# Kernel tuning notes

Measured on AMD Instinct MI355X. Metric: run time of the kernel, lower is better.

The kernel has to match this reference:

```python
import jax, jax.numpy as jnp
from jax import lax
import numpy as np

NODE_COUNT = 4096
BATCH = 128
THRESHOLD = 1.0
DISSIPATION = 0.1
SPARSITY = 0.9
MAX_ITERS = 100


def setup_inputs() -> dict:
    key = jax.random.key(0)
    k_in, k_conn, k_mask, k_w, k_b = jax.random.split(key, 5)
    input_data = jax.random.normal(k_in, (BATCH, NODE_COUNT), dtype=jnp.float32)
    conn = jax.random.normal(k_conn, (NODE_COUNT, NODE_COUNT), dtype=jnp.float32)
    mask = (jax.random.uniform(k_mask, (NODE_COUNT, NODE_COUNT)) > SPARSITY).astype(jnp.float32)
    conn = conn * mask
    conn = conn / (jnp.abs(conn).sum(axis=1, keepdims=True) + 1e-6)
    # input_proj: Linear(node_count, node_count), torch default init scale
    bound = 1.0 / np.sqrt(NODE_COUNT)
    W = jax.random.uniform(k_w, (NODE_COUNT, NODE_COUNT), minval=-bound, maxval=bound, dtype=jnp.float32)
    b = jax.random.uniform(k_b, (NODE_COUNT,), minval=-bound, maxval=bound, dtype=jnp.float32)
    return {"input_data": input_data, "W": W, "b": b, "connections": conn}


def _avalanche(state, connections):
    """Batched avalanche scan with per-sample sticky early-exit (torch break)."""
    B = state.shape[0]
    done0 = jnp.zeros((B,), dtype=bool)
    total0 = jnp.zeros((B,), dtype=state.dtype)

    def step(carry, _):
        state, done, total = carry
        active = (state > THRESHOLD).astype(state.dtype)          # [B, N]
        n_active = active.sum(axis=1)                              # [B]
        new_done = done | (n_active == 0)                          # break condition
        total = total + jnp.where(new_done, 0.0, n_active)
        # propagated = connections @ active  (per sample)
        prop = jnp.einsum('ij,bj->bi', connections, active)        # [B, N]
        new_state = (state * (1.0 - DISSIPATION) + prop * (1.0 - active)) * (1.0 - active)
        state = jnp.where(new_done[:, None], state, new_state)
        return (state, new_done, total), None

    (state, done, total), _ = lax.scan(step, (state, done0, total0), None, length=MAX_ITERS)
    return state, total


def reference(input_data, W, b, connections):
    projected = input_data @ W.T + b                               # [B, N]
    output, sizes = _avalanche(projected, connections)
    max_size = sizes.max()
    return output, max_size
```

## Files before the change

kernel.cpp:

```cpp
#include <hip/hip_runtime.h>

#define N_NODES 4096
#define BATCH 128
#define SPLITK 8
#define GBN 32
#define PITCH 40
#define KCHUNK (N_NODES / SPLITK)
#define NIT (KCHUNK / 32)
#define GEMM_BLOCKS ((N_NODES / GBN) * SPLITK)
#define TRANS_BLOCKS (64 * 64)

typedef _Float16 f16x4 __attribute__((ext_vector_type(4)));
typedef _Float16 f16x8 __attribute__((ext_vector_type(8)));
typedef float f32x4 __attribute__((ext_vector_type(4)));

#if defined(__has_builtin)
#if __has_builtin(__builtin_amdgcn_cvt_f32_fp8) && __has_builtin(__builtin_amdgcn_cvt_pk_fp8_f32)
#define CONN_FP8 1
#endif
#endif
#ifndef CONN_FP8
#define CONN_FP8 0
#endif

#if CONN_FP8
#define CONN_ELEM_BYTES 1
#define CONN_SCALE (1.0f / 256.0f)
#else
#define CONN_ELEM_BYTES 2
#define CONN_SCALE 1.0f
#endif

__device__ __forceinline__ void conn_store4(void* out, size_t off, float4 v) {
#if CONN_FP8
  unsigned int p = __builtin_amdgcn_cvt_pk_fp8_f32(v.x * 256.0f, v.y * 256.0f, 0, false);
  p = (unsigned int)__builtin_amdgcn_cvt_pk_fp8_f32(v.z * 256.0f, v.w * 256.0f, (int)p, true);
  *(unsigned int*)((unsigned char*)out + off) = p;
#else
  const unsigned int ux = __float_as_uint(v.x), uy = __float_as_uint(v.y);
  const unsigned int uz = __float_as_uint(v.z), uw = __float_as_uint(v.w);
  ushort4 u;
  u.x = (unsigned short)((ux + 0x7FFFu + ((ux >> 16) & 1u)) >> 16);
  u.y = (unsigned short)((uy + 0x7FFFu + ((uy >> 16) & 1u)) >> 16);
  u.z = (unsigned short)((uz + 0x7FFFu + ((uz >> 16) & 1u)) >> 16);
  u.w = (unsigned short)((uw + 0x7FFFu + ((uw >> 16) & 1u)) >> 16);
  *(ushort4*)((unsigned short*)out + off) = u;
#endif
}

__device__ __forceinline__ float4 conn_load4(const void* cT, int j, int t) {
#if CONN_FP8
  const unsigned int c = *(const unsigned int*)((const unsigned char*)cT + ((size_t)j << 12) + t * 4);
  return make_float4(__builtin_amdgcn_cvt_f32_fp8(c, 0), __builtin_amdgcn_cvt_f32_fp8(c, 1),
                     __builtin_amdgcn_cvt_f32_fp8(c, 2), __builtin_amdgcn_cvt_f32_fp8(c, 3));
#else
  const ushort4 c = *(const ushort4*)((const unsigned short*)cT + ((size_t)j << 12) + t * 4);
  return make_float4(__uint_as_float((unsigned int)c.x << 16),
                     __uint_as_float((unsigned int)c.y << 16),
                     __uint_as_float((unsigned int)c.z << 16),
                     __uint_as_float((unsigned int)c.w << 16));
#endif
}

struct GemmSmem {
  alignas(16) _Float16 Ah[2][128 * PITCH];
  alignas(16) _Float16 Al[2][128 * PITCH];
  alignas(16) _Float16 Bh[2][GBN * PITCH];
  alignas(16) _Float16 Bl[2][GBN * PITCH];
};
struct TransSmem { float tile[64][65]; };
union PrepSmem { GemmSmem g; TransSmem t; };

__global__ __launch_bounds__(256) void fused_prep_kernel(const float* __restrict__ A,
                                                         const float* __restrict__ W,
                                                         const float* __restrict__ conn,
                                                         float* __restrict__ P,
                                                         void* __restrict__ connT,
                                                         unsigned int* __restrict__ maxslot) {
  __shared__ PrepSmem sm;
  const int tid = threadIdx.x;
  const int bid = blockIdx.x;

  if (bid < GEMM_BLOCKS) {
    if (bid == 0 && tid == 0) *maxslot = 0u;
    const int wave = tid >> 6, lane = tid & 63;
    const int wm = wave >> 1, wn = wave & 1;
    const int g = lane >> 4, lrow = lane & 15;
    const int n0 = (bid & 127) * GBN;
    const int kb = (bid >> 7) * KCHUNK;
    const int srow = tid >> 3;
    const int scol = (tid & 7) * 4;

    const float* Abase = A + (size_t)srow * N_NODES + kb + scol;
    const float* Wbase = W + (size_t)(n0 + srow) * N_NODES + kb + scol;

    f32x4 acc[4] = {};
    float4 avA[4], avB[4], wvA, wvB;
#pragma unroll
    for (int r = 0; r < 4; ++r) avA[r] = *(const float4*)(Abase + (size_t)(r * 32) * N_NODES);
    wvA = *(const float4*)Wbase;
#pragma unroll
    for (int r = 0; r < 4; ++r) avB[r] = *(const float4*)(Abase + (size_t)(r * 32) * N_NODES + 32);
    wvB = *(const float4*)(Wbase + 32);

    auto step = [&](float4 (&av)[4], float4& wv, int buf, int it) {
#pragma unroll
      for (int r = 0; r < 4; ++r) {
        const int row = srow + r * 32;
        f16x4 hi, lo;
        const float x0 = av[r].x * 256.f, x1 = av[r].y * 256.f,
                    x2 = av[r].z * 256.f, x3 = av[r].w * 256.f;
        hi[0] = (_Float16)x0; lo[0] = (_Float16)(x0 - (float)hi[0]);
        hi[1] = (_Float16)x1; lo[1] = (_Float16)(x1 - (float)hi[1]);
        hi[2] = (_Float16)x2; lo[2] = (_Float16)(x2 - (float)hi[2]);
        hi[3] = (_Float16)x3; lo[3] = (_Float16)(x3 - (float)hi[3]);
        *(f16x4*)&sm.g.Ah[buf][row * PITCH + scol] = hi;
        *(f16x4*)&sm.g.Al[buf][row * PITCH + scol] = lo;
      }
      {
        f16x4 hi, lo;
        const float x0 = wv.x * 64.f, x1 = wv.y * 64.f, x2 = wv.z * 64.f, x3 = wv.w * 64.f;
        hi[0] = (_Float16)x0; lo[0] = (_Float16)(x0 - (float)hi[0]);
        hi[1] = (_Float16)x1; lo[1] = (_Float16)(x1 - (float)hi[1]);
        hi[2] = (_Float16)x2; lo[2] = (_Float16)(x2 - (float)hi[2]);
        hi[3] = (_Float16)x3; lo[3] = (_Float16)(x3 - (float)hi[3]);
        *(f16x4*)&sm.g.Bh[buf][srow * PITCH + scol] = hi;
        *(f16x4*)&sm.g.Bl[buf][srow * PITCH + scol] = lo;
      }
      const int knext = ((it + 2) * 32) & (KCHUNK - 1);
#pragma unroll
      for (int r = 0; r < 4; ++r)
        av[r] = *(const float4*)(Abase + (size_t)(r * 32) * N_NODES + knext);
      wv = *(const float4*)(Wbase + knext);

      __syncthreads();

      f16x8 ah[4], al[4], bh, bl;
#pragma unroll
      for (int fm = 0; fm < 4; ++fm) {
        const int m = wm * 64 + fm * 16 + lrow;
        ah[fm] = *(const f16x8*)&sm.g.Ah[buf][m * PITCH + g * 8];
        al[fm] = *(const f16x8*)&sm.g.Al[buf][m * PITCH + g * 8];
      }
      const int nn = wn * 16 + lrow;
      bh = *(const f16x8*)&sm.g.Bh[buf][nn * PITCH + g * 8];
      bl = *(const f16x8*)&sm.g.Bl[buf][nn * PITCH + g * 8];
#pragma unroll
      for (int fm = 0; fm < 4; ++fm) {
        acc[fm] = __builtin_amdgcn_mfma_f32_16x16x32_f16(ah[fm], bh, acc[fm], 0, 0, 0);
        acc[fm] = __builtin_amdgcn_mfma_f32_16x16x32_f16(ah[fm], bl, acc[fm], 0, 0, 0);
        acc[fm] = __builtin_amdgcn_mfma_f32_16x16x32_f16(al[fm], bh, acc[fm], 0, 0, 0);
      }
    };

#pragma unroll
    for (int it = 0; it < NIT; it += 2) {
      step(avA, wvA, 0, it);
      step(avB, wvB, 1, it + 1);
    }

    constexpr float INV = 1.0f / 16384.0f;
    float* Pb = P + (size_t)(bid >> 7) * BATCH * N_NODES;
    const int n = n0 + wn * 16 + lrow;
#pragma unroll
    for (int fm = 0; fm < 4; ++fm)
#pragma unroll
      for (int reg = 0; reg < 4; ++reg) {
        const int m = wm * 64 + fm * 16 + g * 4 + reg;
        Pb[(size_t)m * N_NODES + n] = acc[fm][reg] * INV;
      }
  } else {
    const int idx = bid - GEMM_BLOCKS;
    const int bx = idx & 63, by = idx >> 6;
    const int tx = tid & 15, ty = tid >> 4;
#pragma unroll
    for (int r = 0; r < 4; ++r) {
      const float4 v =
          *(const float4*)(conn + (size_t)(by * 64 + ty + 16 * r) * N_NODES + bx * 64 + tx * 4);
      sm.t.tile[ty + 16 * r][tx * 4 + 0] = v.x;
      sm.t.tile[ty + 16 * r][tx * 4 + 1] = v.y;
      sm.t.tile[ty + 16 * r][tx * 4 + 2] = v.z;
      sm.t.tile[ty + 16 * r][tx * 4 + 3] = v.w;
    }
    __syncthreads();
#pragma unroll
    for (int r = 0; r < 4; ++r) {
      const int orow = ty + 16 * r;
      float4 v;
      v.x = sm.t.tile[tx * 4 + 0][orow];
      v.y = sm.t.tile[tx * 4 + 1][orow];
      v.z = sm.t.tile[tx * 4 + 2][orow];
      v.w = sm.t.tile[tx * 4 + 3][orow];
      conn_store4(connT, (size_t)(bx * 64 + orow) * N_NODES + by * 64 + tx * 4, v);
    }
  }
}

__global__ __launch_bounds__(256) void proj_gemm_valu(const float* __restrict__ A,
                                                      const float* __restrict__ W,
                                                      float* __restrict__ P,
                                                      unsigned int* __restrict__ maxslot) {
  if (blockIdx.x == 0 && threadIdx.x == 0) *maxslot = 0u;
  __shared__ float As[16][132];
  __shared__ float Bs[16][68];
  const int tid = threadIdx.x;
  const int n0 = blockIdx.x * 64;
  const int tx = tid & 15, ty = tid >> 4;
  const int arow = tid >> 1, acol = (tid & 1) * 8;
  const int brow = tid >> 2, bcol = (tid & 3) * 4;
  float acc[2][4][4] = {};
  const float* Aptr = A + (size_t)arow * N_NODES + acol;
  const float* Wptr = W + (size_t)(n0 + brow) * N_NODES + bcol;
  for (int k0 = 0; k0 < N_NODES; k0 += 16) {
    const float4 a0 = *(const float4*)(Aptr + k0);
    const float4 a1 = *(const float4*)(Aptr + k0 + 4);
    const float4 bv = *(const float4*)(Wptr + k0);
    __syncthreads();
    As[acol + 0][arow] = a0.x; As[acol + 1][arow] = a0.y;
    As[acol + 2][arow] = a0.z; As[acol + 3][arow] = a0.w;
    As[acol + 4][arow] = a1.x; As[acol + 5][arow] = a1.y;
    As[acol + 6][arow] = a1.z; As[acol + 7][arow] = a1.w;
    Bs[bcol + 0][brow] = bv.x; Bs[bcol + 1][brow] = bv.y;
    Bs[bcol + 2][brow] = bv.z; Bs[bcol + 3][brow] = bv.w;
    __syncthreads();
#pragma unroll
    for (int kk = 0; kk < 16; ++kk) {
      const float4 av0 = *(const float4*)&As[kk][ty * 4];
      const float4 av1 = *(const float4*)&As[kk][64 + ty * 4];
      const float4 bv4 = *(const float4*)&Bs[kk][tx * 4];
      const float am[8] = {av0.x, av0.y, av0.z, av0.w, av1.x, av1.y, av1.z, av1.w};
      const float bn[4] = {bv4.x, bv4.y, bv4.z, bv4.w};
#pragma unroll
      for (int i2 = 0; i2 < 2; ++i2)
#pragma unroll
        for (int i = 0; i < 4; ++i)
#pragma unroll
          for (int j = 0; j < 4; ++j)
            acc[i2][i][j] += am[i2 * 4 + i] * bn[j];
    }
  }
#pragma unroll
  for (int i2 = 0; i2 < 2; ++i2)
#pragma unroll
    for (int i = 0; i < 4; ++i) {
      const int m = i2 * 64 + ty * 4 + i;
      *(float4*)(P + (size_t)m * N_NODES + n0 + tx * 4) =
          make_float4(acc[i2][i][0], acc[i2][i][1], acc[i2][i][2], acc[i2][i][3]);
    }
}

__global__ __launch_bounds__(256) void bias_inplace_kernel(float* __restrict__ P,
                                                           const float* __restrict__ bias) {
  const size_t base = ((size_t)blockIdx.x * 256 + threadIdx.x) * 4;
  const int n = (int)(base & (N_NODES - 1));
  float4 s = *(const float4*)(P + base);
  const float4 bv = *(const float4*)(bias + n);
  s.x += bv.x; s.y += bv.y; s.z += bv.z; s.w += bv.w;
  *(float4*)(P + base) = s;
}

template <int MODE, int NSPLIT>
__global__ __launch_bounds__(1024) void avalanche_kernel(const float* __restrict__ Pin,
                                                         const float* __restrict__ bias,
                                                         const void* __restrict__ connv,
                                                         float* __restrict__ out,
                                                         unsigned int* __restrict__ maxslot) {
  const int b = blockIdx.x;
  const int t = threadIdx.x;
  __shared__ unsigned long long mask[64];
  __shared__ int wincl[64];
  __shared__ int list[N_NODES];

  float4 s;
  if (MODE == 1) {
    const float4 bv = *(const float4*)(bias + t * 4);
    s = bv;
#pragma unroll
    for (int sp = 0; sp < NSPLIT; ++sp) {
      const float4 v = *(const float4*)(Pin + (size_t)sp * BATCH * N_NODES +
                                        (size_t)b * N_NODES + t * 4);
      s.x += v.x; s.y += v.y; s.z += v.z; s.w += v.w;
    }
  } else {
    s = *(const float4*)(Pin + (size_t)b * N_NODES + t * 4);
  }

  float total = 0.0f;

  for (int it = 0; it < 100; ++it) {
    const float v0 = s.x, v1 = s.y, v2 = s.z, v3 = s.w;
    unsigned int bits = 0;
    if (v0 > 1.0f) bits |= 1u;
    if (v1 > 1.0f) bits |= 2u;
    if (v2 > 1.0f) bits |= 4u;
    if (v3 > 1.0f) bits |= 8u;

    __syncthreads();
    if (t < 64) mask[t] = 0ULL;
    __syncthreads();
    if (bits) atomicOr(&mask[t >> 4], (unsigned long long)bits << ((t & 15) * 4));
    __syncthreads();

    if (t < 64) {
      int incl = __popcll(mask[t]);
#pragma unroll
      for (int d = 1; d < 64; d <<= 1) {
        const int y = __shfl_up(incl, d);
        if (t >= d) incl += y;
      }
      wincl[t] = incl;
    }
    __syncthreads();
    const int n = wincl[63];
    if (n == 0) break;
    total += (float)n;

    if (t < 64) {
      unsigned long long m = mask[t];
      int o = wincl[t] - __popcll(m);
      while (m) {
        list[o++] = (t << 6) + __builtin_ctzll(m);
        m &= m - 1;
      }
    }
    __syncthreads();

    float4 a0 = make_float4(0.f, 0.f, 0.f, 0.f), a1 = a0, a2 = a0, a3 = a0;
    if (MODE == 1) {
      int idx = 0;
      for (; idx + 8 <= n; idx += 8) {
        const float4 c0 = conn_load4(connv, list[idx + 0], t);
        const float4 c1 = conn_load4(connv, list[idx + 1], t);
        const float4 c2 = conn_load4(connv, list[idx + 2], t);
        const float4 c3 = conn_load4(connv, list[idx + 3], t);
        const float4 c4 = conn_load4(connv, list[idx + 4], t);
        const float4 c5 = conn_load4(connv, list[idx + 5], t);
        const float4 c6 = conn_load4(connv, list[idx + 6], t);
        const float4 c7 = conn_load4(connv, list[idx + 7], t);
        a0.x += c0.x; a0.y += c0.y; a0.z += c0.z; a0.w += c0.w;
        a1.x += c1.x; a1.y += c1.y; a1.z += c1.z; a1.w += c1.w;
        a2.x += c2.x; a2.y += c2.y; a2.z += c2.z; a2.w += c2.w;
        a3.x += c3.x; a3.y += c3.y; a3.z += c3.z; a3.w += c3.w;
        a0.x += c4.x; a0.y += c4.y; a0.z += c4.z; a0.w += c4.w;
        a1.x += c5.x; a1.y += c5.y; a1.z += c5.z; a1.w += c5.w;
        a2.x += c6.x; a2.y += c6.y; a2.z += c6.z; a2.w += c6.w;
        a3.x += c7.x; a3.y += c7.y; a3.z += c7.z; a3.w += c7.w;
      }
      for (; idx < n; ++idx) {
        const float4 c = conn_load4(connv, list[idx], t);
        a0.x += c.x; a0.y += c.y; a0.z += c.z; a0.w += c.w;
      }
    } else {
      const float* conn = (const float*)connv;
      for (int idx = 0; idx < n; ++idx) {
        const int j = list[idx];
        a0.x += conn[(size_t)(t * 4 + 0) * N_NODES + j];
        a0.y += conn[(size_t)(t * 4 + 1) * N_NODES + j];
        a0.z += conn[(size_t)(t * 4 + 2) * N_NODES + j];
        a0.w += conn[(size_t)(t * 4 + 3) * N_NODES + j];
      }
    }
    const float sc = (MODE == 1) ? CONN_SCALE : 1.0f;
    const float4 acc = make_float4(((a0.x + a1.x) + (a2.x + a3.x)) * sc,
                                   ((a0.y + a1.y) + (a2.y + a3.y)) * sc,
                                   ((a0.z + a1.z) + (a2.z + a3.z)) * sc,
                                   ((a0.w + a1.w) + (a2.w + a3.w)) * sc);

    s.x = (v0 > 1.0f) ? 0.0f : 0.9f * v0 + acc.x;
    s.y = (v1 > 1.0f) ? 0.0f : 0.9f * v1 + acc.y;
    s.z = (v2 > 1.0f) ? 0.0f : 0.9f * v2 + acc.z;
    s.w = (v3 > 1.0f) ? 0.0f : 0.9f * v3 + acc.w;
  }

  *(float4*)(out + (size_t)b * N_NODES + t * 4) = s;
  if (t == 0) atomicMax(maxslot, __float_as_uint(total));
}

extern "C" void kernel_launch(void* const* d_in, const int* in_sizes, int n_in,
                              void* d_out, int out_size, void* d_ws, size_t ws_size,
                              hipStream_t stream) {
  const float* input = (const float*)d_in[0];
  const float* W     = (const float*)d_in[1];
  const float* bias  = (const float*)d_in[2];
  const float* conn  = (const float*)d_in[3];
  float* out = (float*)d_out;

  const size_t connT_bytes = (size_t)N_NODES * N_NODES * CONN_ELEM_BYTES;
  const size_t part_bytes  = (size_t)SPLITK * BATCH * N_NODES * sizeof(float);
  unsigned int* maxslot = (unsigned int*)(out + (size_t)BATCH * N_NODES);

  if (ws_size >= connT_bytes + part_bytes) {
    void* connT = d_ws;
    float* part = (float*)((char*)d_ws + connT_bytes);
    fused_prep_kernel<<<GEMM_BLOCKS + TRANS_BLOCKS, 256, 0, stream>>>(input, W, conn, part,
                                                                      connT, maxslot);
    avalanche_kernel<1, SPLITK><<<BATCH, 1024, 0, stream>>>(part, bias, connT, out, maxslot);
  } else {
    proj_gemm_valu<<<dim3(N_NODES / 64, 1), 256, 0, stream>>>(input, W, out, maxslot);
    bias_inplace_kernel<<<BATCH * N_NODES / 1024, 256, 0, stream>>>(out, bias);
    avalanche_kernel<0, 1><<<BATCH, 1024, 0, stream>>>(out, nullptr, conn, out, maxslot);
  }
}
```

Measured before the change: 64.36 us.

## Use 64-wide K tiles, single LDS buffer, and interleave GEMM with transpose blocks

The split-K projection GEMM now stages 64-wide K tiles instead of 32, so each barrier pair feeds twice as many MFMAs, and the LDS buffers drop from double to single buffering with a leading barrier. Block assignment is remapped so every fifth block is a GEMM block and the rest do the connection transpose, spreading the heavier GEMM work across CUs instead of front-loading it. The trade-off is higher register pressure from doubling the prefetched float4 registers, which may reduce occupancy.

```diff
diff --git a/kernel.cpp b/kernel.cpp
--- a/kernel.cpp
+++ b/kernel.cpp
@@ -4,9 +4,9 @@
 #define BATCH 128
 #define SPLITK 8
 #define GBN 32
-#define PITCH 40
+#define GBK 64
+#define PITCH 72
 #define KCHUNK (N_NODES / SPLITK)
-#define NIT (KCHUNK / 32)
 #define GEMM_BLOCKS ((N_NODES / GBN) * SPLITK)
 #define TRANS_BLOCKS (64 * 64)
 
@@ -63,10 +63,10 @@
 }
 
 struct GemmSmem {
-  alignas(16) _Float16 Ah[2][128 * PITCH];
-  alignas(16) _Float16 Al[2][128 * PITCH];
-  alignas(16) _Float16 Bh[2][GBN * PITCH];
-  alignas(16) _Float16 Bl[2][GBN * PITCH];
+  alignas(16) _Float16 Ah[128 * PITCH];
+  alignas(16) _Float16 Al[128 * PITCH];
+  alignas(16) _Float16 Bh[GBN * PITCH];
+  alignas(16) _Float16 Bl[GBN * PITCH];
 };
 struct TransSmem { float tile[64][65]; };
 union PrepSmem { GemmSmem g; TransSmem t; };
@@ -81,86 +81,98 @@
   const int tid = threadIdx.x;
   const int bid = blockIdx.x;
 
-  if (bid < GEMM_BLOCKS) {
-    if (bid == 0 && tid == 0) *maxslot = 0u;
+  if (bid % 5 == 0) {
+    const int gb = bid / 5;
+    if (gb == 0 && tid == 0) *maxslot = 0u;
     const int wave = tid >> 6, lane = tid & 63;
     const int wm = wave >> 1, wn = wave & 1;
     const int g = lane >> 4, lrow = lane & 15;
-    const int n0 = (bid & 127) * GBN;
-    const int kb = (bid >> 7) * KCHUNK;
-    const int srow = tid >> 3;
-    const int scol = (tid & 7) * 4;
-
-    const float* Abase = A + (size_t)srow * N_NODES + kb + scol;
-    const float* Wbase = W + (size_t)(n0 + srow) * N_NODES + kb + scol;
+    const int n0 = (gb & 127) * GBN;
+    const int kb = (gb >> 7) * KCHUNK;
+    const int ar = tid >> 4;
+    const int ac = (tid & 15) * 4;
+    const int wr = tid >> 3;
+    const int wc = (tid & 7) * 4;
+
+    const float* Abase = A + (size_t)ar * N_NODES + kb + ac;
+    const float* Wbase = W + (size_t)(n0 + wr) * N_NODES + kb + wc;
 
     f32x4 acc[4] = {};
-    float4 avA[4], avB[4], wvA, wvB;
-#pragma unroll
-    for (int r = 0; r < 4; ++r) avA[r] = *(const float4*)(Abase + (size_t)(r * 32) * N_NODES);
-    wvA = *(const float4*)Wbase;
-#pragma unroll
-    for (int r = 0; r < 4; ++r) avB[r] = *(const float4*)(Abase + (size_t)(r * 32) * N_NODES + 32);
-    wvB = *(const float4*)(Wbase + 32);
-
-    auto step = [&](float4 (&av)[4], float4& wv, int buf, int it) {
-#pragma unroll
-      for (int r = 0; r < 4; ++r) {
-        const int row = srow + r * 32;
+    float4 avA[8], avB[8], wvA[2], wvB[2];
+#pragma unroll
+    for (int i = 0; i < 8; ++i) avA[i] = *(const float4*)(Abase + (size_t)(16 * i) * N_NODES);
+#pragma unroll
+    for (int i = 0; i < 2; ++i) wvA[i] = *(const float4*)(Wbase + 32 * i);
+#pragma unroll
+    for (int i = 0; i < 8; ++i) avB[i] = *(const float4*)(Abase + (size_t)(16 * i) * N_NODES + GBK);
+#pragma unroll
+    for (int i = 0; i < 2; ++i) wvB[i] = *(const float4*)(Wbase + 32 * i + GBK);
+
+    auto step = [&](float4 (&av)[8], float4 (&wv)[2], int knext) {
+      __syncthreads();
+#pragma unroll
+      for (int i = 0; i < 8; ++i) {
+        const int row = ar + 16 * i;
         f16x4 hi, lo;
-        const float x0 = av[r].x * 256.f, x1 = av[r].y * 256.f,
-                    x2 = av[r].z * 256.f, x3 = av[r].w * 256.f;
+        const float x0 = av[i].x * 256.f, x1 = av[i].y * 256.f,
+                    x2 = av[i].z * 256.f, x3 = av[i].w * 256.f;
         hi[0] = (_Float16)x0; lo[0] = (_Float16)(x0 - (float)hi[0]);
         hi[1] = (_Float16)x1; lo[1] = (_Float16)(x1 - (float)hi[1]);
         hi[2] = (_Float16)x2; lo[2] = (_Float16)(x2 - (float)hi[2]);
         hi[3] = (_Float16)x3; lo[3] = (_Float16)(x3 - (float)hi[3]);
-        *(f16x4*)&sm.g.Ah[buf][row * PITCH + scol] = hi;
-        *(f16x4*)&sm.g.Al[buf][row * PITCH + scol] = lo;
-      }
-      {
+        *(f16x4*)&sm.g.Ah[row * PITCH + ac] = hi;
+        *(f16x4*)&sm.g.Al[row * PITCH + ac] = lo;
+      }
+#pragma unroll
+      for (int i = 0; i < 2; ++i) {
         f16x4 hi, lo;
-        const float x0 = wv.x * 64.f, x1 = wv.y * 64.f, x2 = wv.z * 64.f, x3 = wv.w * 64.f;
+        const float x0 = wv[i].x * 64.f, x1 = wv[i].y * 64.f,
+                    x2 = wv[i].z * 64.f, x3 = wv[i].w * 64.f;
         hi[0] = (_Float16)x0; lo[0] = (_Float16)(x0 - (float)hi[0]);
         hi[1] = (_Float16)x1; lo[1] = (_Float16)(x1 - (float)hi[1]);
         hi[2] = (_Float16)x2; lo[2] = (_Float16)(x2 - (float)hi[2]);
         hi[3] = (_Float16)x3; lo[3] = (_Float16)(x3 - (float)hi[3]);
-        *(f16x4*)&sm.g.Bh[buf][srow * PITCH + scol] = hi;
-        *(f16x4*)&sm.g.Bl[buf][srow * PITCH + scol] = lo;
-      }
-      const int knext = ((it + 2) * 32) & (KCHUNK - 1);
-#pragma unroll
-      for (int r = 0; r < 4; ++r)
-        av[r] = *(const float4*)(Abase + (size_t)(r * 32) * N_NODES + knext);
-      wv = *(const float4*)(Wbase + knext);
+        *(f16x4*)&sm.g.Bh[wr * PITCH + wc + 32 * i] = hi;
+        *(f16x4*)&sm.g.Bl[wr * PITCH + wc + 32 * i] = lo;
+      }
+#pragma unroll
+      for (int i = 0; i < 8; ++i)
+        av[i] = *(const float4*)(Abase + (size_t)(16 * i) * N_NODES + knext);
+#pragma unroll
+      for (int i = 0; i < 2; ++i) wv[i] = *(const float4*)(Wbase + 32 * i + knext);
 
       __syncthreads();
 
-      f16x8 ah[4], al[4], bh, bl;
-#pragma unroll
-      for (int fm = 0; fm < 4; ++fm) {
-        const int m = wm * 64 + fm * 16 + lrow;
-        ah[fm] = *(const f16x8*)&sm.g.Ah[buf][m * PITCH + g * 8];
-        al[fm] = *(const f16x8*)&sm.g.Al[buf][m * PITCH + g * 8];
-      }
-      const int nn = wn * 16 + lrow;
-      bh = *(const f16x8*)&sm.g.Bh[buf][nn * PITCH + g * 8];
-      bl = *(const f16x8*)&sm.g.Bl[buf][nn * PITCH + g * 8];
-#pragma unroll
-      for (int fm = 0; fm < 4; ++fm) {
-        acc[fm] = __builtin_amdgcn_mfma_f32_16x16x32_f16(ah[fm], bh, acc[fm], 0, 0, 0);
-        acc[fm] = __builtin_amdgcn_mfma_f32_16x16x32_f16(ah[fm], bl, acc[fm], 0, 0, 0);
-        acc[fm] = __builtin_amdgcn_mfma_f32_16x16x32_f16(al[fm], bh, acc[fm], 0, 0, 0);
+#pragma unroll
+      for (int kk = 0; kk < 2; ++kk) {
+        const int ko = kk * 32 + g * 8;
+        f16x8 ah[4], al[4], bh, bl;
+#pragma unroll
+        for (int fm = 0; fm < 4; ++fm) {
+          const int m = wm * 64 + fm * 16 + lrow;
+          ah[fm] = *(const f16x8*)&sm.g.Ah[m * PITCH + ko];
+          al[fm] = *(const f16x8*)&sm.g.Al[m * PITCH + ko];
+        }
+        const int nn = wn * 16 + lrow;
+        bh = *(const f16x8*)&sm.g.Bh[nn * PITCH + ko];
+        bl = *(const f16x8*)&sm.g.Bl[nn * PITCH + ko];
+#pragma unroll
+        for (int fm = 0; fm < 4; ++fm) {
+          acc[fm] = __builtin_amdgcn_mfma_f32_16x16x32_f16(ah[fm], bh, acc[fm], 0, 0, 0);
+          acc[fm] = __builtin_amdgcn_mfma_f32_16x16x32_f16(ah[fm], bl, acc[fm], 0, 0, 0);
+          acc[fm] = __builtin_amdgcn_mfma_f32_16x16x32_f16(al[fm], bh, acc[fm], 0, 0, 0);
+        }
       }
     };
 
 #pragma unroll
-    for (int it = 0; it < NIT; it += 2) {
-      step(avA, wvA, 0, it);
-      step(avB, wvB, 1, it + 1);
+    for (int it = 0; it < KCHUNK / GBK; it += 2) {
+      step(avA, wvA, ((it + 2) * GBK) & (KCHUNK - 1));
+      step(avB, wvB, ((it + 3) * GBK) & (KCHUNK - 1));
     }
 
     constexpr float INV = 1.0f / 16384.0f;
-    float* Pb = P + (size_t)(bid >> 7) * BATCH * N_NODES;
+    float* Pb = P + (size_t)(gb >> 7) * BATCH * N_NODES;
     const int n = n0 + wn * 16 + lrow;
 #pragma unroll
     for (int fm = 0; fm < 4; ++fm)
@@ -170,7 +182,7 @@
         Pb[(size_t)m * N_NODES + n] = acc[fm][reg] * INV;
       }
   } else {
-    const int idx = bid - GEMM_BLOCKS;
+    const int idx = bid - bid / 5 - 1;
     const int bx = idx & 63, by = idx >> 6;
     const int tx = tid & 15, ty = tid >> 4;
 #pragma unroll
```

Result: slower. 69.96 us (+8.7%).

## Pre-split A into fp16 planes and stream GEMM tiles via global-to-LDS DMA

Applied to the files above, without the earlier changes.

A new small kernel converts the input activations to fp16 hi/lo planes once, so the projection GEMM no longer redoes the split in every N-block. The GEMM main loop now loads A planes and raw fp32 W tiles straight into XOR-swizzled LDS with global_load_lds, and the W hi/lo split happens at fragment-read time. The K tile grows to 64 and the double buffering is replaced by one buffer with an issue-after-compute pattern. This adds a kernel launch and an extra workspace round trip, and the single buffer leaves no overlap between loads and MFMA.

```diff
diff --git a/kernel.cpp b/kernel.cpp
--- a/kernel.cpp
+++ b/kernel.cpp
@@ -4,15 +4,25 @@
 #define BATCH 128
 #define SPLITK 8
 #define GBN 32
-#define PITCH 40
+#define GBK 64
 #define KCHUNK (N_NODES / SPLITK)
-#define NIT (KCHUNK / 32)
+#define NSTEP (KCHUNK / GBK)
 #define GEMM_BLOCKS ((N_NODES / GBN) * SPLITK)
 #define TRANS_BLOCKS (64 * 64)
 
 typedef _Float16 f16x4 __attribute__((ext_vector_type(4)));
 typedef _Float16 f16x8 __attribute__((ext_vector_type(8)));
 typedef float f32x4 __attribute__((ext_vector_type(4)));
+typedef unsigned int u32x4 __attribute__((ext_vector_type(4)));
+
+__device__ __forceinline__ void dma16(const void* g, void* l) {
+#if defined(__has_builtin) && __has_builtin(__builtin_amdgcn_global_load_lds)
+  __builtin_amdgcn_global_load_lds((const __attribute__((address_space(1))) void*)g,
+                                   (__attribute__((address_space(3))) void*)l, 16, 0, 0);
+#else
+  *(u32x4*)l = *(const u32x4*)g;
+#endif
+}
 
 #if defined(__has_builtin)
 #if __has_builtin(__builtin_amdgcn_cvt_f32_fp8) && __has_builtin(__builtin_amdgcn_cvt_pk_fp8_f32)
@@ -62,101 +72,110 @@
 #endif
 }
 
+__global__ __launch_bounds__(256) void asplit_kernel(const float* __restrict__ in,
+                                                     _Float16* __restrict__ Ah,
+                                                     _Float16* __restrict__ Al,
+                                                     unsigned int* __restrict__ maxslot) {
+  if (blockIdx.x == 0 && threadIdx.x == 0) *maxslot = 0u;
+  const size_t idx = ((size_t)blockIdx.x * 256 + threadIdx.x) * 4;
+  const float4 v = *(const float4*)(in + idx);
+  f16x4 hi, lo;
+  const float x0 = v.x * 256.f, x1 = v.y * 256.f, x2 = v.z * 256.f, x3 = v.w * 256.f;
+  hi[0] = (_Float16)x0; lo[0] = (_Float16)(x0 - (float)hi[0]);
+  hi[1] = (_Float16)x1; lo[1] = (_Float16)(x1 - (float)hi[1]);
+  hi[2] = (_Float16)x2; lo[2] = (_Float16)(x2 - (float)hi[2]);
+  hi[3] = (_Float16)x3; lo[3] = (_Float16)(x3 - (float)hi[3]);
+  *(f16x4*)(Ah + idx) = hi;
+  *(f16x4*)(Al + idx) = lo;
+}
+
 struct GemmSmem {
-  alignas(16) _Float16 Ah[2][128 * PITCH];
-  alignas(16) _Float16 Al[2][128 * PITCH];
-  alignas(16) _Float16 Bh[2][GBN * PITCH];
-  alignas(16) _Float16 Bl[2][GBN * PITCH];
+  alignas(16) _Float16 Ah[128 * GBK];
+  alignas(16) _Float16 Al[128 * GBK];
+  alignas(16) float B[GBN * GBK];
 };
 struct TransSmem { float tile[64][65]; };
 union PrepSmem { GemmSmem g; TransSmem t; };
 
-__global__ __launch_bounds__(256) void fused_prep_kernel(const float* __restrict__ A,
-                                                         const float* __restrict__ W,
-                                                         const float* __restrict__ conn,
-                                                         float* __restrict__ P,
-                                                         void* __restrict__ connT,
-                                                         unsigned int* __restrict__ maxslot) {
+__global__ __launch_bounds__(256, 4) void fused_prep_kernel(
+    const _Float16* __restrict__ Ah, const _Float16* __restrict__ Al,
+    const float* __restrict__ W, const float* __restrict__ conn,
+    float* __restrict__ P, void* __restrict__ connT) {
   __shared__ PrepSmem sm;
   const int tid = threadIdx.x;
   const int bid = blockIdx.x;
 
   if (bid < GEMM_BLOCKS) {
-    if (bid == 0 && tid == 0) *maxslot = 0u;
     const int wave = tid >> 6, lane = tid & 63;
     const int wm = wave >> 1, wn = wave & 1;
     const int g = lane >> 4, lrow = lane & 15;
     const int n0 = (bid & 127) * GBN;
     const int kb = (bid >> 7) * KCHUNK;
-    const int srow = tid >> 3;
-    const int scol = (tid & 7) * 4;
-
-    const float* Abase = A + (size_t)srow * N_NODES + kb + scol;
-    const float* Wbase = W + (size_t)(n0 + srow) * N_NODES + kb + scol;
+
+    const char* AsrcBase = (const char*)((wave >> 1) ? Al : Ah);
+    _Float16* AldsBase = (wave >> 1) ? sm.g.Al : sm.g.Ah;
+    const int ac0 = (wave & 1) * 8;
+    const int arow_l = lane >> 3;
+    const int ainrow = (((lane & 7) << 4) ^ ((lane >> 3) << 4));
+    const int brow_l = lane >> 4;
+    const int binrow0 = (lane & 15) << 4;
+
+    auto issue = [&](int t) {
+      const size_t kbyteA = (size_t)(kb + t * GBK) * 2;
+      const size_t kbyteB = (size_t)(kb + t * GBK) * 4;
+#pragma unroll
+      for (int i = 0; i < 8; ++i) {
+        const int c = ac0 + i;
+        const int row = 8 * c + arow_l;
+        dma16(AsrcBase + (size_t)row * (N_NODES * 2) + kbyteA + ainrow,
+              (char*)AldsBase + c * 1024 + lane * 16);
+      }
+#pragma unroll
+      for (int i = 0; i < 2; ++i) {
+        const int c = wave * 2 + i;
+        const int row = 4 * c + brow_l;
+        dma16((const char*)W + (size_t)(n0 + row) * (N_NODES * 4) + kbyteB +
+                  (binrow0 ^ ((row & 7) << 4)),
+              (char*)sm.g.B + c * 1024 + lane * 16);
+      }
+    };
 
     f32x4 acc[4] = {};
-    float4 avA[4], avB[4], wvA, wvB;
-#pragma unroll
-    for (int r = 0; r < 4; ++r) avA[r] = *(const float4*)(Abase + (size_t)(r * 32) * N_NODES);
-    wvA = *(const float4*)Wbase;
-#pragma unroll
-    for (int r = 0; r < 4; ++r) avB[r] = *(const float4*)(Abase + (size_t)(r * 32) * N_NODES + 32);
-    wvB = *(const float4*)(Wbase + 32);
-
-    auto step = [&](float4 (&av)[4], float4& wv, int buf, int it) {
-#pragma unroll
-      for (int r = 0; r < 4; ++r) {
-        const int row = srow + r * 32;
-        f16x4 hi, lo;
-        const float x0 = av[r].x * 256.f, x1 = av[r].y * 256.f,
-                    x2 = av[r].z * 256.f, x3 = av[r].w * 256.f;
-        hi[0] = (_Float16)x0; lo[0] = (_Float16)(x0 - (float)hi[0]);
-        hi[1] = (_Float16)x1; lo[1] = (_Float16)(x1 - (float)hi[1]);
-        hi[2] = (_Float16)x2; lo[2] = (_Float16)(x2 - (float)hi[2]);
-        hi[3] = (_Float16)x3; lo[3] = (_Float16)(x3 - (float)hi[3]);
-        *(f16x4*)&sm.g.Ah[buf][row * PITCH + scol] = hi;
-        *(f16x4*)&sm.g.Al[buf][row * PITCH + scol] = lo;
-      }
-      {
-        f16x4 hi, lo;
-        const float x0 = wv.x * 64.f, x1 = wv.y * 64.f, x2 = wv.z * 64.f, x3 = wv.w * 64.f;
-        hi[0] = (_Float16)x0; lo[0] = (_Float16)(x0 - (float)hi[0]);
-        hi[1] = (_Float16)x1; lo[1] = (_Float16)(x1 - (float)hi[1]);
-        hi[2] = (_Float16)x2; lo[2] = (_Float16)(x2 - (float)hi[2]);
-        hi[3] = (_Float16)x3; lo[3] = (_Float16)(x3 - (float)hi[3]);
-        *(f16x4*)&sm.g.Bh[buf][srow * PITCH + scol] = hi;
-        *(f16x4*)&sm.g.Bl[buf][srow * PITCH + scol] = lo;
-      }
-      const int knext = ((it + 2) * 32) & (KCHUNK - 1);
-#pragma unroll
-      for (int r = 0; r < 4; ++r)
-        av[r] = *(const float4*)(Abase + (size_t)(r * 32) * N_NODES + knext);
-      wv = *(const float4*)(Wbase + knext);
-
+    issue(0);
+    for (int t = 0; t < NSTEP; ++t) {
       __syncthreads();
-
-      f16x8 ah[4], al[4], bh, bl;
-#pragma unroll
-      for (int fm = 0; fm < 4; ++fm) {
-        const int m = wm * 64 + fm * 16 + lrow;
-        ah[fm] = *(const f16x8*)&sm.g.Ah[buf][m * PITCH + g * 8];
-        al[fm] = *(const f16x8*)&sm.g.Al[buf][m * PITCH + g * 8];
-      }
-      const int nn = wn * 16 + lrow;
-      bh = *(const f16x8*)&sm.g.Bh[buf][nn * PITCH + g * 8];
-      bl = *(const f16x8*)&sm.g.Bl[buf][nn * PITCH + g * 8];
-#pragma unroll
-      for (int fm = 0; fm < 4; ++fm) {
-        acc[fm] = __builtin_amdgcn_mfma_f32_16x16x32_f16(ah[fm], bh, acc[fm], 0, 0, 0);
-        acc[fm] = __builtin_amdgcn_mfma_f32_16x16x32_f16(ah[fm], bl, acc[fm], 0, 0, 0);
-        acc[fm] = __builtin_amdgcn_mfma_f32_16x16x32_f16(al[fm], bh, acc[fm], 0, 0, 0);
-      }
-    };
-
-#pragma unroll
-    for (int it = 0; it < NIT; it += 2) {
-      step(avA, wvA, 0, it);
-      step(avB, wvB, 1, it + 1);
+#pragma unroll
+      for (int kk = 0; kk < 2; ++kk) {
+        const int br = wn * 16 + lrow;
+        const char* bbase = (const char*)sm.g.B + br * 256;
+        const int bm = (br & 7) << 4;
+        const int cb = (kk * 32 + g * 8) * 4;
+        const f32x4 b0 = *(const f32x4*)(bbase + ((cb) ^ bm));
+        const f32x4 b1 = *(const f32x4*)(bbase + ((cb + 16) ^ bm));
+        f16x8 bh, bl;
+#pragma unroll
+        for (int j = 0; j < 4; ++j) {
+          const float x = b0[j] * 64.f;
+          const _Float16 h = (_Float16)x;
+          bh[j] = h; bl[j] = (_Float16)(x - (float)h);
+          const float y = b1[j] * 64.f;
+          const _Float16 h2 = (_Float16)y;
+          bh[4 + j] = h2; bl[4 + j] = (_Float16)(y - (float)h2);
+        }
+#pragma unroll
+        for (int fm = 0; fm < 4; ++fm) {
+          const int ar = wm * 64 + fm * 16 + lrow;
+          const int am = (ar & 7) << 4;
+          const int ca = (kk * 32 + g * 8) * 2;
+          const f16x8 ah = *(const f16x8*)((const char*)sm.g.Ah + ar * 128 + (ca ^ am));
+          const f16x8 al = *(const f16x8*)((const char*)sm.g.Al + ar * 128 + (ca ^ am));
+          acc[fm] = __builtin_amdgcn_mfma_f32_16x16x32_f16(ah, bh, acc[fm], 0, 0, 0);
+          acc[fm] = __builtin_amdgcn_mfma_f32_16x16x32_f16(ah, bl, acc[fm], 0, 0, 0);
+          acc[fm] = __builtin_amdgcn_mfma_f32_16x16x32_f16(al, bh, acc[fm], 0, 0, 0);
+        }
+      }
+      __syncthreads();
+      if (t + 1 < NSTEP) issue(t + 1);
     }
 
     constexpr float INV = 1.0f / 16384.0f;
@@ -385,15 +404,19 @@
   const float* conn  = (const float*)d_in[3];
   float* out = (float*)d_out;
 
-  const size_t connT_bytes = (size_t)N_NODES * N_NODES * CONN_ELEM_BYTES;
-  const size_t part_bytes  = (size_t)SPLITK * BATCH * N_NODES * sizeof(float);
+  const size_t aplane_bytes = (size_t)BATCH * N_NODES * 2;
+  const size_t connT_bytes  = (size_t)N_NODES * N_NODES * CONN_ELEM_BYTES;
+  const size_t part_bytes   = (size_t)SPLITK * BATCH * N_NODES * sizeof(float);
   unsigned int* maxslot = (unsigned int*)(out + (size_t)BATCH * N_NODES);
 
-  if (ws_size >= connT_bytes + part_bytes) {
-    void* connT = d_ws;
-    float* part = (float*)((char*)d_ws + connT_bytes);
-    fused_prep_kernel<<<GEMM_BLOCKS + TRANS_BLOCKS, 256, 0, stream>>>(input, W, conn, part,
-                                                                      connT, maxslot);
+  if (ws_size >= 2 * aplane_bytes + connT_bytes + part_bytes) {
+    _Float16* Ah = (_Float16*)d_ws;
+    _Float16* Al = (_Float16*)((char*)d_ws + aplane_bytes);
+    void* connT  = (char*)d_ws + 2 * aplane_bytes;
+    float* part  = (float*)((char*)d_ws + 2 * aplane_bytes + connT_bytes);
+    asplit_kernel<<<BATCH * N_NODES / 1024, 256, 0, stream>>>(input, Ah, Al, maxslot);
+    fused_prep_kernel<<<GEMM_BLOCKS + TRANS_BLOCKS, 256, 0, stream>>>(Ah, Al, W, conn, part,
+                                                                      connT);
     avalanche_kernel<1, SPLITK><<<BATCH, 1024, 0, stream>>>(part, bias, connT, out, maxslot);
   } else {
     proj_gemm_valu<<<dim3(N_NODES / 64, 1), 256, 0, stream>>>(input, W, out, maxslot);
```

Result: slower. 67.91 us (+5.5%).
